# Kernel optimization log

Measured on AMD Instinct MI355X. Metric: run time of the kernel, lower is better.

The kernel has to match this reference:

```python
import jax, jax.numpy as jnp
import numpy as np
from jax import lax

MODEL_DIM = 384
KERNEL = 15
PAD = (KERNEL - 1) // 2
BATCH = 4096


def fake_quant(x, bits):
    """Per-tensor symmetric fake quantization with straight-through estimator.
    scale = max|x| / qmax, q = clip(round(x/scale), qmin, qmax), dq = q*scale.
    """
    qmax = float(2 ** (bits - 1) - 1)
    qmin = -float(2 ** (bits - 1))
    scale = jnp.maximum(jnp.max(jnp.abs(x)) / qmax, jnp.asarray(1e-8, x.dtype))
    dq = jnp.clip(jnp.round(x / scale), qmin, qmax) * scale
    return x + lax.stop_gradient(dq - x)  # STE: identity gradient


def setup_inputs() -> dict:
    key = jax.random.key(0)
    k = jax.random.split(key, 7)
    image = jax.random.normal(k[0], (BATCH, 28, 28), dtype=jnp.float32)
    # LinearQuant(28 -> model_dim)
    W1 = jax.random.normal(k[1], (MODEL_DIM, 28), dtype=jnp.float32) * (1.0 / np.sqrt(28))
    b1 = jax.random.normal(k[2], (MODEL_DIM,), dtype=jnp.float32) * 0.01
    # depthwise Conv1DQuant(model_dim, model_dim, K, groups=model_dim): weight [C_out, 1, K]
    Wc = jax.random.normal(k[3], (MODEL_DIM, 1, KERNEL), dtype=jnp.float32) * (1.0 / np.sqrt(KERNEL))
    bc = jax.random.normal(k[4], (MODEL_DIM,), dtype=jnp.float32) * 0.01
    # LinearQuant(28*model_dim -> 10)
    Wf = jax.random.normal(k[5], (10, 28 * MODEL_DIM), dtype=jnp.float32) * (1.0 / np.sqrt(28 * MODEL_DIM))
    bf = jax.random.normal(k[6], (10,), dtype=jnp.float32) * 0.01
    return {"image": image, "W1": W1, "b1": b1, "Wc": Wc, "bc": bc, "Wf": Wf, "bf": bf}


def reference(image, W1, b1, Wc, bc, Wf, bf):
    inp = image.reshape(-1, 28, 28)
    # linear_1 with 8-bit activation fake-quant in and 3-bit weight fake-quant
    x = fake_quant(inp, 8)
    lin = jnp.einsum('blf,of->blo', x, fake_quant(W1, 3)) + b1  # [B,28,model_dim]
    out1 = jnp.tanh(fake_quant(lin, 8))
    # depthwise conv1d over length 28, channels model_dim
    xc = jnp.transpose(fake_quant(out1, 8), (0, 2, 1))  # [B,C,L]
    conv = lax.conv_general_dilated(
        xc, fake_quant(Wc, 3), window_strides=(1,), padding=[(PAD, PAD)],
        dimension_numbers=('NCH', 'OIH', 'NCH'), feature_group_count=MODEL_DIM)
    conv = conv + bc[None, :, None]                      # [B,C,L]
    conv = jnp.transpose(conv, (0, 2, 1))                # [B,L,C]
    out2 = jnp.tanh(fake_quant(conv, 8)).reshape(-1, MODEL_DIM * 28)
    # final linear
    logits = fake_quant(out2, 8) @ fake_quant(Wf, 3).T + bf  # [B,10]
    return fake_quant(logits, 8)
```

## Files before the change

kernel.cpp:

```cpp
#include <hip/hip_runtime.h>

#define BATCH 4096
#define MD 384
#define KW 15
#define PADW 7
#define LSEQ 28
#define FIN 28

#define NX (BATCH*LSEQ*FIN)


#define B_SCF  0
#define B_LUT1 256
#define B_LUT2 512
#define B_PT0  1024
#define B_PT1  33792
#define B_PT2  41984
#define B_PTL  50176
#define B_W1B  54272
#define B_WCQ  78848
#define B_WFB  84992
#define B_LG   257024
#define B_XQB  420864

typedef __bf16 bf16x8 __attribute__((ext_vector_type(8)));
typedef float f32x4 __attribute__((ext_vector_type(4)));
typedef int i32x4 __attribute__((ext_vector_type(4)));

#if __has_builtin(__builtin_amdgcn_sdot4)
#define SDOT4(a,b,c) __builtin_amdgcn_sdot4((a),(b),(c),false)
#else
__device__ __forceinline__ int SDOT4(int a,int b,int c){
  c += ((a<<24)>>24)*((b<<24)>>24);
  c += ((a<<16)>>24)*((b<<16)>>24);
  c += ((a<<8)>>24)*((b<<8)>>24);
  c += (a>>24)*(b>>24);
  return c;
}
#endif

#if __has_builtin(__builtin_amdgcn_alignbyte)
#define ALIGNB(hi,lo,s) __builtin_amdgcn_alignbyte((hi),(lo),(s))
#else
#define ALIGNB(hi,lo,s) ((int)(((unsigned)(lo)>>(8*(s)))|((unsigned)(hi)<<(32-8*(s)))))
#endif

__device__ __forceinline__ unsigned short f2bf(float f){
  return (unsigned short)(__float_as_uint(f)>>16);
}

__device__ __forceinline__ unsigned lut_bperm(int iw,int lutw){
  int res=__builtin_amdgcn_ds_bpermute(iw,lutw);
  return ((unsigned)res>>(8*(iw&3)))&0xFFu;
}

__device__ __forceinline__ void blkStore4(float m0,float m1,float m2,float m3,float4* dst){
  #pragma unroll
  for(int off=32;off;off>>=1){
    m0=fmaxf(m0,__shfl_xor(m0,off,64));
    m1=fmaxf(m1,__shfl_xor(m1,off,64));
    m2=fmaxf(m2,__shfl_xor(m2,off,64));
    m3=fmaxf(m3,__shfl_xor(m3,off,64));
  }
  __shared__ float sm[4][4];
  int wid=threadIdx.x>>6;
  if((threadIdx.x&63)==0){sm[wid][0]=m0;sm[wid][1]=m1;sm[wid][2]=m2;sm[wid][3]=m3;}
  __syncthreads();
  if(threadIdx.x==0){
    for(int i=1;i<4;i++){
      m0=fmaxf(m0,sm[i][0]);m1=fmaxf(m1,sm[i][1]);
      m2=fmaxf(m2,sm[i][2]);m3=fmaxf(m3,sm[i][3]);
    }
    *dst=make_float4(m0,m1,m2,m3);
  }
}

__device__ __forceinline__ void blkStoreMM(float mn,float mx,float2* dst){
  #pragma unroll
  for(int off=32;off;off>>=1){
    mn=fminf(mn,__shfl_xor(mn,off,64));
    mx=fmaxf(mx,__shfl_xor(mx,off,64));
  }
  __shared__ float smn[8],smx[8];
  int wid=threadIdx.x>>6, nw=blockDim.x>>6;
  if((threadIdx.x&63)==0){smn[wid]=mn;smx[wid]=mx;}
  __syncthreads();
  if(threadIdx.x==0){
    for(int i=1;i<nw;i++){mn=fminf(mn,smn[i]);mx=fmaxf(mx,smx[i]);}
    *dst=make_float2(mn,mx);
  }
}

__global__ __launch_bounds__(256)
void k_maxabs_in(const float* __restrict__ img,const float* __restrict__ W1,
                 const float* __restrict__ Wc,const float* __restrict__ Wf,
                 float4* __restrict__ pt0){
  float m0=0.f,m1=0.f,m2=0.f,m3=0.f;
  const int N4=NX/4;
  const int NW1=MD*FIN, NWC=MD*KW, NWF=10*MD*LSEQ;
  const int total=N4+NW1+NWC+NWF;
  const float4* img4=(const float4*)img;
  for(int i=blockIdx.x*blockDim.x+threadIdx.x;i<total;i+=gridDim.x*blockDim.x){
    if(i<N4){
      float4 v=img4[i];
      m0=fmaxf(m0,fmaxf(fmaxf(fabsf(v.x),fabsf(v.y)),fmaxf(fabsf(v.z),fabsf(v.w))));
    }
    else if(i<N4+NW1) m1=fmaxf(m1,fabsf(W1[i-N4]));
    else if(i<N4+NW1+NWC) m2=fmaxf(m2,fabsf(Wc[i-N4-NW1]));
    else m3=fmaxf(m3,fabsf(Wf[i-N4-NW1-NWC]));
  }
  blkStore4(m0,m1,m2,m3,&pt0[blockIdx.x]);
}

__global__ __launch_bounds__(256)
void k_red0(const float4* __restrict__ pt,float* __restrict__ scf){
  int t=threadIdx.x;
  float m0=0.f,m1=0.f,m2=0.f,m3=0.f;
  for(int i=t;i<2048;i+=256){
    float4 v=pt[i];
    m0=fmaxf(m0,v.x);m1=fmaxf(m1,v.y);m2=fmaxf(m2,v.z);m3=fmaxf(m3,v.w);
  }
  #pragma unroll
  for(int off=32;off;off>>=1){
    m0=fmaxf(m0,__shfl_xor(m0,off,64));
    m1=fmaxf(m1,__shfl_xor(m1,off,64));
    m2=fmaxf(m2,__shfl_xor(m2,off,64));
    m3=fmaxf(m3,__shfl_xor(m3,off,64));
  }
  __shared__ float sm[4][4];
  int wid=t>>6;
  if((t&63)==0){sm[wid][0]=m0;sm[wid][1]=m1;sm[wid][2]=m2;sm[wid][3]=m3;}
  __syncthreads();
  if(t==0){
    for(int i=1;i<4;i++){
      m0=fmaxf(m0,sm[i][0]);m1=fmaxf(m1,sm[i][1]);
      m2=fmaxf(m2,sm[i][2]);m3=fmaxf(m3,sm[i][3]);
    }
    scf[0]=fmaxf(m0/127.f,1e-8f);
    scf[1]=fmaxf(m1/3.f,1e-8f);
    scf[2]=fmaxf(m2/3.f,1e-8f);
    scf[3]=fmaxf(m3/3.f,1e-8f);
  }
}

__global__ __launch_bounds__(256)
void k_redmm(const float2* __restrict__ pt,int n,float* __restrict__ scf,
             int preIdx,int outIdx,char* __restrict__ lutg){
  int t=threadIdx.x;
  float mn=1e30f,mx=-1e30f;
  for(int i=t;i<n;i+=256){
    float2 v=pt[i];
    mn=fminf(mn,v.x); mx=fmaxf(mx,v.y);
  }
  #pragma unroll
  for(int off=32;off;off>>=1){
    mn=fminf(mn,__shfl_xor(mn,off,64));
    mx=fmaxf(mx,__shfl_xor(mx,off,64));
  }
  __shared__ float smn[4],smx[4];
  __shared__ float bs,bso;
  int wid=t>>6;
  if((t&63)==0){smn[wid]=mn;smx[wid]=mx;}
  __syncthreads();
  if(t==0){
    for(int i=1;i<4;i++){mn=fminf(mn,smn[i]);mx=fmaxf(mx,smx[i]);}
    float ma=fmaxf(fabsf(mn),fabsf(mx));
    float s=fmaxf(ma/127.f,1e-8f);
    float a1=fabsf(fminf(fmaxf(rintf(mn/s),-128.f),127.f)*s);
    float a2=fabsf(fminf(fmaxf(rintf(mx/s),-128.f),127.f)*s);
    float so=fmaxf(tanhf(fmaxf(a1,a2))/127.f,1e-8f);
    scf[preIdx]=s; scf[outIdx]=so;
    bs=s; bso=so;
  }
  __syncthreads();
  float d=(float)(t-128)*bs;
  lutg[t]=(char)(int)fminf(fmaxf(rintf(tanhf(d)/bso),-128.f),127.f);
}

__global__ __launch_bounds__(256)
void k_prep(const float* __restrict__ img,const float* __restrict__ W1,
            const float* __restrict__ Wc,const float* __restrict__ Wf,
            const float* __restrict__ scf,char* __restrict__ wsb){
  float s_img=scf[0], s_w1=scf[1], s_wc=scf[2], s_wf=scf[3];
  float inv_img=1.f/s_img;
  unsigned short* xqb=(unsigned short*)(wsb+B_XQB);
  unsigned short* w1b=(unsigned short*)(wsb+B_W1B);
  char* wcpk=wsb+B_WCQ;
  char* wfb=wsb+B_WFB;
  const int T0=BATCH*LSEQ*32;
  const int T1=T0+MD*32;
  const int T2=T1+MD*16;
  const int T3=T2+10*10752;
  for(int i=blockIdx.x*blockDim.x+threadIdx.x;i<T3;i+=gridDim.x*blockDim.x){
    if(i<T0){
      int row=i>>5, cc=i&31;
      float q = cc<FIN ? fminf(fmaxf(rintf(img[row*FIN+cc]*inv_img),-128.f),127.f) : 0.f;
      xqb[i]=f2bf(q);
    } else if(i<T1){
      int j=i-T0; int o=j>>5, cc=j&31;
      float q = cc<FIN ? fminf(fmaxf(rintf(W1[o*FIN+cc]/s_w1),-4.f),3.f) : 0.f;
      w1b[j]=f2bf(q);
    } else if(i<T2){
      int j=i-T1; int c=j>>4, k=j&15;
      char q=0;
      if(k<KW) q=(char)(int)fminf(fmaxf(rintf(Wc[c*KW+k]/s_wc),-4.f),3.f);
      wcpk[j]=q;
    } else {
      int j=i-T2;
      int n=j/10752, r=j-n*10752;
      int c=r/28, l=r-c*28;
      wfb[j]=(char)(int)fminf(fmaxf(rintf(Wf[n*10752+l*MD+c]/s_wf),-4.f),3.f);
    }
  }
}

#define CWS 29
#define DWS 2692
template<int MODE>
__global__ __launch_bounds__(512)
void k_fused(const unsigned short* __restrict__ xqb,const unsigned short* __restrict__ w1b,
             const float* __restrict__ b1,const float* __restrict__ scf,
             const char* __restrict__ lut1g,const char* __restrict__ lut2g,
             const char* __restrict__ wcpk,const float* __restrict__ bc,
             const char* __restrict__ wfb,const float* __restrict__ bfv,
             float2* __restrict__ ptmm,float* __restrict__ lg,
             float* __restrict__ ptl){
  __shared__ int ldsI[MD*CWS];
  __shared__ int psumN[8][10][4];
  int t=threadIdx.x, wid=t>>6, lane=t&63, l4=lane>>4, l15=lane&15;
  {
    const int* src=(const int*)w1b;
    for(int i=t;i<6144;i+=512) ldsI[i]=src[i];
  }
  __syncthreads();
  unsigned short* Wlds=(unsigned short*)ldsI;
  bf16x8 bfr[3]; float b1v[3];
  #pragma unroll
  for(int ni=0;ni<3;ni++){
    int o=(wid*3+ni)*16+l15;
    bfr[ni]=*(const bf16x8*)&Wlds[o*32+l4*8];
    b1v[ni]=b1[o];
  }
  bf16x8 af[7];
  int r0=blockIdx.x*112;
  #pragma unroll
  for(int mt=0;mt<7;mt++)
    af[mt]=*(const bf16x8*)&xqb[(size_t)(r0+mt*16+l15)*32+l4*8];
  float sg=scf[0]*scf[1];
  float sgi=sg, b1s[3]={0.f,0.f,0.f};
  int lutA_w=0,lutB_w=0;
  float ck1=1.f,inv_cv=1.f,sfac=1.f,gsc=1.f;
  if constexpr(MODE>=1){
    float inv_lin=1.f/scf[4];
    sgi=sg*inv_lin;
    #pragma unroll
    for(int ni=0;ni<3;ni++) b1s[ni]=fmaf(b1v[ni],inv_lin,128.f);
    lutA_w=((const int*)lut1g)[lane];
    sfac=scf[5]*scf[2];
  }
  if constexpr(MODE==2){
    inv_cv=1.f/scf[6];
    ck1=sfac*inv_cv;
    gsc=scf[3]*scf[7];
    lutB_w=((const int*)lut2g)[lane];
  }
  if constexpr(MODE>=1) __syncthreads();

  f32x4 zero={0.f,0.f,0.f,0.f};
  float mn=1e30f,mx=-1e30f;
  float mnn[3]={1e30f,1e30f,1e30f},mxx[3]={-1e30f,-1e30f,-1e30f};
  #pragma unroll
  for(int ni=0;ni<3;ni++){
    int o=(wid*3+ni)*16+l15;
    #pragma unroll
    for(int mt=0;mt<7;mt++){
      f32x4 acc=__builtin_amdgcn_mfma_f32_16x16x32_bf16(af[mt],bfr[ni],zero,0,0,0);
      if constexpr(MODE==0){
        #pragma unroll
        for(int r=0;r<4;r++){
          mnn[ni]=fminf(mnn[ni],acc[r]); mxx[ni]=fmaxf(mxx[ni],acc[r]);
        }
      } else {
        unsigned w=0;
        #pragma unroll
        for(int r=0;r<4;r++){
          float x=fmaf(acc[r],sgi,b1s[ni]);
          int iw=(int)__builtin_amdgcn_fmed3f(rintf(x),0.f,255.f);
          w|=lut_bperm(iw,lutA_w)<<(8*r);
        }
        ldsI[o*CWS+mt*4+l4]=(int)w;
      }
    }
  }
  if constexpr(MODE==0){
    #pragma unroll
    for(int ni=0;ni<3;ni++){
      mn=fminf(mn,fmaf(mnn[ni],sg,b1v[ni]));
      mx=fmaxf(mx,fmaf(mxx[ni],sg,b1v[ni]));
    }
    blkStoreMM(mn,mx,&ptmm[blockIdx.x]);
    return;
  }
  __syncthreads();

  int oww[3][7];
  float mnc=1e30f,mxc=-1e30f;
  #pragma unroll
  for(int rr=0;rr<3;rr++){
    int j=t+rr*512;
    int s=j/384, c=j-s*384;
    i32x4 wq=*(const i32x4*)(wcpk+(size_t)c*16);
    float cbias=bc[c];
    float cq2=0.f;
    if constexpr(MODE==2) cq2=fmaf(cbias,inv_cv,128.f);
    int ext[11];
    ext[0]=0; ext[1]=0; ext[9]=0; ext[10]=0;
    #pragma unroll
    for(int i=0;i<7;i++) ext[2+i]=ldsI[c*CWS+s*7+i];
    int imn=0x7FFFFFFF,imx=0x80000000;
    #pragma unroll
    for(int l=0;l<LSEQ;l++){
      const int eb=l+1, bi=eb>>2, sh=eb&3;
      int A0,A1,A2,A3;
      if(sh==0){A0=ext[bi];A1=ext[bi+1];A2=ext[bi+2];A3=ext[bi+3];}
      else{
        A0=ALIGNB(ext[bi+1],ext[bi],sh);
        A1=ALIGNB(ext[bi+2],ext[bi+1],sh);
        A2=ALIGNB(ext[bi+3],ext[bi+2],sh);
        A3=ALIGNB(ext[bi+4],ext[bi+3],sh);
      }
      int idot=SDOT4(A0,wq[0],SDOT4(A1,wq[1],SDOT4(A2,wq[2],SDOT4(A3,wq[3],0))));
      if constexpr(MODE==1){
        imn=min(imn,idot); imx=max(imx,idot);
      } else {
        float x=fmaf((float)idot,ck1,cq2);
        int iw=(int)__builtin_amdgcn_fmed3f(rintf(x),0.f,255.f);
        unsigned q2=lut_bperm(iw,lutB_w);
        if((l&3)==0) oww[rr][l>>2]=(int)q2;
        else oww[rr][l>>2]|=(int)(q2<<(8*(l&3)));
      }
    }
    if constexpr(MODE==1){
      mnc=fminf(mnc,fmaf((float)imn,sfac,cbias));
      mxc=fmaxf(mxc,fmaf((float)imx,sfac,cbias));
    }
  }
  if constexpr(MODE==1){
    blkStoreMM(mnc,mxc,&ptmm[blockIdx.x]);
    return;
  }

  __syncthreads();
  #pragma unroll
  for(int rr=0;rr<3;rr++){
    int j=t+rr*512;
    int s=j/384, c=j-s*384;
    #pragma unroll
    for(int i=0;i<7;i++) ldsI[s*DWS+c*7+i]=oww[rr][i];
  }
  __syncthreads();

  {
    i32x4 acc={0,0,0,0};
    const char* ldsB=(const char*)ldsI;
    for(int kb=wid;kb<168;kb+=8){
      i32x4 a=*(const i32x4*)(ldsB+(size_t)(l15&3)*(DWS*4)+kb*64+l4*16);
      i32x4 b=*(const i32x4*)(wfb+(size_t)l15*10752+kb*64+l4*16);
      acc=__builtin_amdgcn_mfma_i32_16x16x64_i8(a,b,acc,0,0,0);
    }
    if(l4==0&&l15<10){
      #pragma unroll
      for(int r=0;r<4;r++) psumN[wid][l15][r]=acc[r];
    }
  }
  __syncthreads();
  float m=0.f;
  if(t<40){
    int s=t/10, o=t-s*10;
    int sum=0;
    #pragma unroll
    for(int w=0;w<8;w++) sum+=psumN[w][o][s];
    float v=fmaf((float)sum,gsc,bfv[o]);
    lg[(blockIdx.x*4+s)*10+o]=v;
    m=fabsf(v);
  }
  if(t<64){
    #pragma unroll
    for(int off=32;off;off>>=1) m=fmaxf(m,__shfl_xor(m,off,64));
    if(t==0) ptl[blockIdx.x]=m;
  }
}

__global__ __launch_bounds__(256)
void k_final(const float* __restrict__ lg,const float* __restrict__ ptl,
             float* __restrict__ out){
  int t=threadIdx.x;
  float m=0.f;
  for(int i=t;i<1024;i+=256) m=fmaxf(m,ptl[i]);
  #pragma unroll
  for(int off=32;off;off>>=1) m=fmaxf(m,__shfl_xor(m,off,64));
  __shared__ float sm[4];
  __shared__ float sv;
  int wid=t>>6;
  if((t&63)==0) sm[wid]=m;
  __syncthreads();
  if(t==0){
    for(int k=1;k<4;k++) m=fmaxf(m,sm[k]);
    sv=fmaxf(m/127.f,1e-8f);
  }
  __syncthreads();
  float s=sv;
  int i=blockIdx.x*256+t;
  out[i]=fminf(fmaxf(rintf(lg[i]/s),-128.f),127.f)*s;
}

extern "C" void kernel_launch(void* const* d_in, const int* in_sizes, int n_in,
                              void* d_out, int out_size, void* d_ws, size_t ws_size,
                              hipStream_t stream){
  const float* img=(const float*)d_in[0];
  const float* W1 =(const float*)d_in[1];
  const float* b1 =(const float*)d_in[2];
  const float* Wc =(const float*)d_in[3];
  const float* bc =(const float*)d_in[4];
  const float* Wf =(const float*)d_in[5];
  const float* bf =(const float*)d_in[6];
  float* out=(float*)d_out;
  char* wsb=(char*)d_ws;
  float* scf=(float*)(wsb+B_SCF);
  float4* pt0=(float4*)(wsb+B_PT0);
  float2* pt1=(float2*)(wsb+B_PT1);
  float2* pt2=(float2*)(wsb+B_PT2);
  float* ptl=(float*)(wsb+B_PTL);
  float* lg=(float*)(wsb+B_LG);
  const unsigned short* xqb=(const unsigned short*)(wsb+B_XQB);
  const unsigned short* w1b=(const unsigned short*)(wsb+B_W1B);
  const char* wcpk=wsb+B_WCQ;
  const char* wfb=wsb+B_WFB;

  k_maxabs_in<<<2048,256,0,stream>>>(img,W1,Wc,Wf,pt0);
  k_red0<<<1,256,0,stream>>>(pt0,scf);
  k_prep<<<4096,256,0,stream>>>(img,W1,Wc,Wf,scf,wsb);
  k_fused<0><<<1024,512,0,stream>>>(xqb,w1b,b1,scf,nullptr,nullptr,wcpk,bc,wfb,bf,pt1,nullptr,nullptr);
  k_redmm<<<1,256,0,stream>>>(pt1,1024,scf,4,5,wsb+B_LUT1);
  k_fused<1><<<1024,512,0,stream>>>(xqb,w1b,b1,scf,wsb+B_LUT1,nullptr,wcpk,bc,wfb,bf,pt2,nullptr,nullptr);
  k_redmm<<<1,256,0,stream>>>(pt2,1024,scf,6,7,wsb+B_LUT2);
  k_fused<2><<<1024,512,0,stream>>>(xqb,w1b,b1,scf,wsb+B_LUT1,wsb+B_LUT2,wcpk,bc,wfb,bf,nullptr,lg,ptl);
  k_final<<<160,256,0,stream>>>(lg,ptl,out);
}
```

Before: 105.6 us.

## Fold single-block reductions into consumer kernels and halve per-block batch tile

Removes the three single-block reduction kernels (k_red0, two k_redmm). Each consumer block now redoes the global min/max reduction over the partials itself and builds the tanh LUTs in shared memory. Each fused block now handles 2 samples (56 rows) instead of 4, doubling the grid to 2048 blocks and shrinking LDS use for higher occupancy. The trade is redundant reduction and LUT work in every block and lower MFMA utilisation per block, since 64 rows are computed for 56 used and only 2 of 4 result rows in the final matmul.

```diff
diff --git a/kernel.cpp b/kernel.cpp
--- a/kernel.cpp
+++ b/kernel.cpp
@@ -3,25 +3,21 @@
 #define BATCH 4096
 #define MD 384
 #define KW 15
-#define PADW 7
 #define LSEQ 28
 #define FIN 28
-
 #define NX (BATCH*LSEQ*FIN)
-
+#define NROWS (BATCH*LSEQ)
 
 #define B_SCF  0
-#define B_LUT1 256
-#define B_LUT2 512
 #define B_PT0  1024
 #define B_PT1  33792
-#define B_PT2  41984
-#define B_PTL  50176
-#define B_W1B  54272
-#define B_WCQ  78848
-#define B_WFB  84992
-#define B_LG   257024
-#define B_XQB  420864
+#define B_PT2  50176
+#define B_PTL  66560
+#define B_W1B  74752
+#define B_WCQ  99328
+#define B_WFB  105472
+#define B_LG   277504
+#define B_XQB  441344
 
 typedef __bf16 bf16x8 __attribute__((ext_vector_type(8)));
 typedef float f32x4 __attribute__((ext_vector_type(4)));
@@ -48,10 +44,18 @@
 __device__ __forceinline__ unsigned short f2bf(float f){
   return (unsigned short)(__float_as_uint(f)>>16);
 }
-
 __device__ __forceinline__ unsigned lut_bperm(int iw,int lutw){
   int res=__builtin_amdgcn_ds_bpermute(iw,lutw);
   return ((unsigned)res>>(8*(iw&3)))&0xFFu;
+}
+
+__device__ __forceinline__ void derive_scales(float mn,float mx,float* sp,float* so){
+  float ma=fmaxf(fabsf(mn),fabsf(mx));
+  float s=fmaxf(ma/127.f,1e-8f);
+  float a1=fabsf(fminf(fmaxf(rintf(mn/s),-128.f),127.f)*s);
+  float a2=fabsf(fminf(fmaxf(rintf(mx/s),-128.f),127.f)*s);
+  *sp=s;
+  *so=fmaxf(tanhf(fmaxf(a1,a2))/127.f,1e-8f);
 }
 
 __device__ __forceinline__ void blkStore4(float m0,float m1,float m2,float m3,float4* dst){
@@ -113,11 +117,14 @@
 }
 
 __global__ __launch_bounds__(256)
-void k_red0(const float4* __restrict__ pt,float* __restrict__ scf){
+void k_prep(const float* __restrict__ img,const float* __restrict__ W1,
+            const float* __restrict__ Wc,const float* __restrict__ Wf,
+            const float4* __restrict__ pt0,float* __restrict__ scf,
+            char* __restrict__ wsb){
   int t=threadIdx.x;
   float m0=0.f,m1=0.f,m2=0.f,m3=0.f;
   for(int i=t;i<2048;i+=256){
-    float4 v=pt[i];
+    float4 v=pt0[i];
     m0=fmaxf(m0,v.x);m1=fmaxf(m1,v.y);m2=fmaxf(m2,v.z);m3=fmaxf(m3,v.w);
   }
   #pragma unroll
@@ -128,6 +135,7 @@
     m3=fmaxf(m3,__shfl_xor(m3,off,64));
   }
   __shared__ float sm[4][4];
+  __shared__ float bs[4];
   int wid=t>>6;
   if((t&63)==0){sm[wid][0]=m0;sm[wid][1]=m1;sm[wid][2]=m2;sm[wid][3]=m3;}
   __syncthreads();
@@ -136,58 +144,20 @@
       m0=fmaxf(m0,sm[i][0]);m1=fmaxf(m1,sm[i][1]);
       m2=fmaxf(m2,sm[i][2]);m3=fmaxf(m3,sm[i][3]);
     }
-    scf[0]=fmaxf(m0/127.f,1e-8f);
-    scf[1]=fmaxf(m1/3.f,1e-8f);
-    scf[2]=fmaxf(m2/3.f,1e-8f);
-    scf[3]=fmaxf(m3/3.f,1e-8f);
-  }
-}
-
-__global__ __launch_bounds__(256)
-void k_redmm(const float2* __restrict__ pt,int n,float* __restrict__ scf,
-             int preIdx,int outIdx,char* __restrict__ lutg){
-  int t=threadIdx.x;
-  float mn=1e30f,mx=-1e30f;
-  for(int i=t;i<n;i+=256){
-    float2 v=pt[i];
-    mn=fminf(mn,v.x); mx=fmaxf(mx,v.y);
-  }
-  #pragma unroll
-  for(int off=32;off;off>>=1){
-    mn=fminf(mn,__shfl_xor(mn,off,64));
-    mx=fmaxf(mx,__shfl_xor(mx,off,64));
-  }
-  __shared__ float smn[4],smx[4];
-  __shared__ float bs,bso;
-  int wid=t>>6;
-  if((t&63)==0){smn[wid]=mn;smx[wid]=mx;}
-  __syncthreads();
-  if(t==0){
-    for(int i=1;i<4;i++){mn=fminf(mn,smn[i]);mx=fmaxf(mx,smx[i]);}
-    float ma=fmaxf(fabsf(mn),fabsf(mx));
-    float s=fmaxf(ma/127.f,1e-8f);
-    float a1=fabsf(fminf(fmaxf(rintf(mn/s),-128.f),127.f)*s);
-    float a2=fabsf(fminf(fmaxf(rintf(mx/s),-128.f),127.f)*s);
-    float so=fmaxf(tanhf(fmaxf(a1,a2))/127.f,1e-8f);
-    scf[preIdx]=s; scf[outIdx]=so;
-    bs=s; bso=so;
-  }
-  __syncthreads();
-  float d=(float)(t-128)*bs;
-  lutg[t]=(char)(int)fminf(fmaxf(rintf(tanhf(d)/bso),-128.f),127.f);
-}
-
-__global__ __launch_bounds__(256)
-void k_prep(const float* __restrict__ img,const float* __restrict__ W1,
-            const float* __restrict__ Wc,const float* __restrict__ Wf,
-            const float* __restrict__ scf,char* __restrict__ wsb){
-  float s_img=scf[0], s_w1=scf[1], s_wc=scf[2], s_wf=scf[3];
+    bs[0]=fmaxf(m0/127.f,1e-8f);
+    bs[1]=fmaxf(m1/3.f,1e-8f);
+    bs[2]=fmaxf(m2/3.f,1e-8f);
+    bs[3]=fmaxf(m3/3.f,1e-8f);
+    if(blockIdx.x==0){scf[0]=bs[0];scf[1]=bs[1];scf[2]=bs[2];scf[3]=bs[3];}
+  }
+  __syncthreads();
+  float s_img=bs[0], s_w1=bs[1], s_wc=bs[2], s_wf=bs[3];
   float inv_img=1.f/s_img;
   unsigned short* xqb=(unsigned short*)(wsb+B_XQB);
   unsigned short* w1b=(unsigned short*)(wsb+B_W1B);
   char* wcpk=wsb+B_WCQ;
   char* wfb=wsb+B_WFB;
-  const int T0=BATCH*LSEQ*32;
+  const int T0=NROWS*32;
   const int T1=T0+MD*32;
   const int T2=T1+MD*16;
   const int T3=T2+10*10752;
@@ -214,19 +184,22 @@
   }
 }
 
-#define CWS 29
-#define DWS 2692
+#define CWS 15
+#define DWSB 10768
 template<int MODE>
 __global__ __launch_bounds__(512)
 void k_fused(const unsigned short* __restrict__ xqb,const unsigned short* __restrict__ w1b,
              const float* __restrict__ b1,const float* __restrict__ scf,
-             const char* __restrict__ lut1g,const char* __restrict__ lut2g,
+             const float2* __restrict__ pt1,const float2* __restrict__ pt2,
              const char* __restrict__ wcpk,const float* __restrict__ bc,
              const char* __restrict__ wfb,const float* __restrict__ bfv,
-             float2* __restrict__ ptmm,float* __restrict__ lg,
+             float2* __restrict__ ptout,float* __restrict__ lg,
              float* __restrict__ ptl){
-  __shared__ int ldsI[MD*CWS];
-  __shared__ int psumN[8][10][4];
+  __shared__ int ldsI[6144];
+  __shared__ int psumN[8][10][2];
+  __shared__ char lutCA[256];
+  __shared__ char lutCB[256];
+  __shared__ float rs[2][8];
   int t=threadIdx.x, wid=t>>6, lane=t&63, l4=lane>>4, l15=lane&15;
   {
     const int* src=(const int*)w1b;
@@ -241,39 +214,85 @@
     bfr[ni]=*(const bf16x8*)&Wlds[o*32+l4*8];
     b1v[ni]=b1[o];
   }
-  bf16x8 af[7];
-  int r0=blockIdx.x*112;
-  #pragma unroll
-  for(int mt=0;mt<7;mt++)
-    af[mt]=*(const bf16x8*)&xqb[(size_t)(r0+mt*16+l15)*32+l4*8];
+  bf16x8 af[4];
+  int r0=blockIdx.x*56;
+  #pragma unroll
+  for(int mt=0;mt<4;mt++){
+    int rr=r0+mt*16+l15; rr=min(rr,NROWS-1);
+    af[mt]=*(const bf16x8*)&xqb[(size_t)rr*32+l4*8];
+  }
   float sg=scf[0]*scf[1];
   float sgi=sg, b1s[3]={0.f,0.f,0.f};
   int lutA_w=0,lutB_w=0;
   float ck1=1.f,inv_cv=1.f,sfac=1.f,gsc=1.f;
+  float s_lin=1.f,s_o1=1.f,s_cv=1.f,s_o2=1.f;
   if constexpr(MODE>=1){
-    float inv_lin=1.f/scf[4];
+    float mn1=1e30f,mx1=-1e30f;
+    for(int i=t;i<2048;i+=512){float2 v=pt1[i]; mn1=fminf(mn1,v.x); mx1=fmaxf(mx1,v.y);}
+    #pragma unroll
+    for(int off=32;off;off>>=1){
+      mn1=fminf(mn1,__shfl_xor(mn1,off,64));
+      mx1=fmaxf(mx1,__shfl_xor(mx1,off,64));
+    }
+    if(lane==0){rs[0][wid]=mn1; rs[1][wid]=mx1;}
+    __syncthreads();
+    mn1=rs[0][0]; mx1=rs[1][0];
+    #pragma unroll
+    for(int i=1;i<8;i++){mn1=fminf(mn1,rs[0][i]); mx1=fmaxf(mx1,rs[1][i]);}
+    derive_scales(mn1,mx1,&s_lin,&s_o1);
+    float inv_lin=1.f/s_lin;
     sgi=sg*inv_lin;
     #pragma unroll
     for(int ni=0;ni<3;ni++) b1s[ni]=fmaf(b1v[ni],inv_lin,128.f);
-    lutA_w=((const int*)lut1g)[lane];
-    sfac=scf[5]*scf[2];
+    sfac=s_o1*scf[2];
   }
   if constexpr(MODE==2){
-    inv_cv=1.f/scf[6];
+    float mn2=1e30f,mx2=-1e30f;
+    for(int i=t;i<2048;i+=512){float2 v=pt2[i]; mn2=fminf(mn2,v.x); mx2=fmaxf(mx2,v.y);}
+    #pragma unroll
+    for(int off=32;off;off>>=1){
+      mn2=fminf(mn2,__shfl_xor(mn2,off,64));
+      mx2=fmaxf(mx2,__shfl_xor(mx2,off,64));
+    }
+    __syncthreads();
+    if(lane==0){rs[0][wid]=mn2; rs[1][wid]=mx2;}
+    __syncthreads();
+    mn2=rs[0][0]; mx2=rs[1][0];
+    #pragma unroll
+    for(int i=1;i<8;i++){mn2=fminf(mn2,rs[0][i]); mx2=fmaxf(mx2,rs[1][i]);}
+    derive_scales(mn2,mx2,&s_cv,&s_o2);
+    inv_cv=1.f/s_cv;
     ck1=sfac*inv_cv;
-    gsc=scf[3]*scf[7];
-    lutB_w=((const int*)lut2g)[lane];
-  }
-  if constexpr(MODE>=1) __syncthreads();
+    gsc=scf[3]*s_o2;
+  }
+  if constexpr(MODE==1){
+    if(t<256){
+      float d=(float)(t-128)*s_lin;
+      lutCA[t]=(char)(int)fminf(fmaxf(rintf(tanhf(d)/s_o1),-128.f),127.f);
+    }
+  }
+  if constexpr(MODE==2){
+    if(t<256){
+      float d=(float)(t-128)*s_lin;
+      lutCA[t]=(char)(int)fminf(fmaxf(rintf(tanhf(d)/s_o1),-128.f),127.f);
+    } else {
+      float d=(float)(t-384)*s_cv;
+      lutCB[t-256]=(char)(int)fminf(fmaxf(rintf(tanhf(d)/s_o2),-128.f),127.f);
+    }
+  }
+  if constexpr(MODE>=1){
+    __syncthreads();
+    lutA_w=((const int*)lutCA)[lane];
+    if constexpr(MODE==2) lutB_w=((const int*)lutCB)[lane];
+  }
 
   f32x4 zero={0.f,0.f,0.f,0.f};
-  float mn=1e30f,mx=-1e30f;
   float mnn[3]={1e30f,1e30f,1e30f},mxx[3]={-1e30f,-1e30f,-1e30f};
   #pragma unroll
   for(int ni=0;ni<3;ni++){
     int o=(wid*3+ni)*16+l15;
     #pragma unroll
-    for(int mt=0;mt<7;mt++){
+    for(int mt=0;mt<4;mt++){
       f32x4 acc=__builtin_amdgcn_mfma_f32_16x16x32_bf16(af[mt],bfr[ni],zero,0,0,0);
       if constexpr(MODE==0){
         #pragma unroll
@@ -288,75 +307,84 @@
           int iw=(int)__builtin_amdgcn_fmed3f(rintf(x),0.f,255.f);
           w|=lut_bperm(iw,lutA_w)<<(8*r);
         }
-        ldsI[o*CWS+mt*4+l4]=(int)w;
+        int idx=mt*4+l4;
+        if(idx<14) ldsI[o*CWS+idx]=(int)w;
       }
     }
   }
   if constexpr(MODE==0){
+    float mn=1e30f,mx=-1e30f;
     #pragma unroll
     for(int ni=0;ni<3;ni++){
       mn=fminf(mn,fmaf(mnn[ni],sg,b1v[ni]));
       mx=fmaxf(mx,fmaf(mxx[ni],sg,b1v[ni]));
     }
-    blkStoreMM(mn,mx,&ptmm[blockIdx.x]);
+    blkStoreMM(mn,mx,&ptout[blockIdx.x]);
     return;
   }
   __syncthreads();
 
-  int oww[3][7];
+  int oww[2][7];
   float mnc=1e30f,mxc=-1e30f;
   #pragma unroll
-  for(int rr=0;rr<3;rr++){
+  for(int rr=0;rr<2;rr++){
     int j=t+rr*512;
-    int s=j/384, c=j-s*384;
-    i32x4 wq=*(const i32x4*)(wcpk+(size_t)c*16);
-    float cbias=bc[c];
-    float cq2=0.f;
-    if constexpr(MODE==2) cq2=fmaf(cbias,inv_cv,128.f);
-    int ext[11];
-    ext[0]=0; ext[1]=0; ext[9]=0; ext[10]=0;
-    #pragma unroll
-    for(int i=0;i<7;i++) ext[2+i]=ldsI[c*CWS+s*7+i];
-    int imn=0x7FFFFFFF,imx=0x80000000;
-    #pragma unroll
-    for(int l=0;l<LSEQ;l++){
-      const int eb=l+1, bi=eb>>2, sh=eb&3;
-      int A0,A1,A2,A3;
-      if(sh==0){A0=ext[bi];A1=ext[bi+1];A2=ext[bi+2];A3=ext[bi+3];}
-      else{
-        A0=ALIGNB(ext[bi+1],ext[bi],sh);
-        A1=ALIGNB(ext[bi+2],ext[bi+1],sh);
-        A2=ALIGNB(ext[bi+3],ext[bi+2],sh);
-        A3=ALIGNB(ext[bi+4],ext[bi+3],sh);
+    if(j<768){
+      int s=j>>8>=1?(j>=384?1:0):(j>=384?1:0);
+      s=(j>=384)?1:0;
+      int c=j-s*384;
+      i32x4 wq=*(const i32x4*)(wcpk+(size_t)c*16);
+      float cbias=bc[c];
+      float cq2=0.f;
+      if constexpr(MODE==2) cq2=fmaf(cbias,inv_cv,128.f);
+      int ext[11];
+      ext[0]=0; ext[1]=0; ext[9]=0; ext[10]=0;
+      #pragma unroll
+      for(int i=0;i<7;i++) ext[2+i]=ldsI[c*CWS+s*7+i];
+      int imn=0x7FFFFFFF,imx=0x80000000;
+      #pragma unroll
+      for(int l=0;l<LSEQ;l++){
+        const int eb=l+1, bi=eb>>2, sh=eb&3;
+        int A0,A1,A2,A3;
+        if(sh==0){A0=ext[bi];A1=ext[bi+1];A2=ext[bi+2];A3=ext[bi+3];}
+        else{
+          A0=ALIGNB(ext[bi+1],ext[bi],sh);
+          A1=ALIGNB(ext[bi+2],ext[bi+1],sh);
+          A2=ALIGNB(ext[bi+3],ext[bi+2],sh);
+          A3=ALIGNB(ext[bi+4],ext[bi+3],sh);
+        }
+        int idot=SDOT4(A0,wq[0],SDOT4(A1,wq[1],SDOT4(A2,wq[2],SDOT4(A3,wq[3],0))));
+        if constexpr(MODE==1){
+          imn=min(imn,idot); imx=max(imx,idot);
+        } else {
+          float x=fmaf((float)idot,ck1,cq2);
+          int iw=(int)__builtin_amdgcn_fmed3f(rintf(x),0.f,255.f);
+          unsigned q2=lut_bperm(iw,lutB_w);
+          if((l&3)==0) oww[rr][l>>2]=(int)q2;
+          else oww[rr][l>>2]|=(int)(q2<<(8*(l&3)));
+        }
       }
-      int idot=SDOT4(A0,wq[0],SDOT4(A1,wq[1],SDOT4(A2,wq[2],SDOT4(A3,wq[3],0))));
       if constexpr(MODE==1){
-        imn=min(imn,idot); imx=max(imx,idot);
-      } else {
-        float x=fmaf((float)idot,ck1,cq2);
-        int iw=(int)__builtin_amdgcn_fmed3f(rintf(x),0.f,255.f);
-        unsigned q2=lut_bperm(iw,lutB_w);
-        if((l&3)==0) oww[rr][l>>2]=(int)q2;
-        else oww[rr][l>>2]|=(int)(q2<<(8*(l&3)));
+        mnc=fminf(mnc,fmaf((float)imn,sfac,cbias));
+        mxc=fmaxf(mxc,fmaf((float)imx,sfac,cbias));
       }
     }
-    if constexpr(MODE==1){
-      mnc=fminf(mnc,fmaf((float)imn,sfac,cbias));
-      mxc=fmaxf(mxc,fmaf((float)imx,sfac,cbias));
-    }
   }
   if constexpr(MODE==1){
-    blkStoreMM(mnc,mxc,&ptmm[blockIdx.x]);
+    blkStoreMM(mnc,mxc,&ptout[blockIdx.x]);
     return;
   }
 
   __syncthreads();
   #pragma unroll
-  for(int rr=0;rr<3;rr++){
+  for(int rr=0;rr<2;rr++){
     int j=t+rr*512;
-    int s=j/384, c=j-s*384;
-    #pragma unroll
-    for(int i=0;i<7;i++) ldsI[s*DWS+c*7+i]=oww[rr][i];
+    if(j<768){
+      int s=(j>=384)?1:0;
+      int c=j-s*384;
+      #pragma unroll
+      for(int i=0;i<7;i++) ldsI[s*(DWSB/4)+c*7+i]=oww[rr][i];
+    }
   }
   __syncthreads();
 
@@ -364,24 +392,24 @@
     i32x4 acc={0,0,0,0};
     const char* ldsB=(const char*)ldsI;
     for(int kb=wid;kb<168;kb+=8){
-      i32x4 a=*(const i32x4*)(ldsB+(size_t)(l15&3)*(DWS*4)+kb*64+l4*16);
+      i32x4 a=*(const i32x4*)(ldsB+(size_t)(l15&1)*DWSB+kb*64+l4*16);
       i32x4 b=*(const i32x4*)(wfb+(size_t)l15*10752+kb*64+l4*16);
       acc=__builtin_amdgcn_mfma_i32_16x16x64_i8(a,b,acc,0,0,0);
     }
     if(l4==0&&l15<10){
-      #pragma unroll
-      for(int r=0;r<4;r++) psumN[wid][l15][r]=acc[r];
+      psumN[wid][l15][0]=acc[0];
+      psumN[wid][l15][1]=acc[1];
     }
   }
   __syncthreads();
   float m=0.f;
-  if(t<40){
+  if(t<20){
     int s=t/10, o=t-s*10;
     int sum=0;
     #pragma unroll
     for(int w=0;w<8;w++) sum+=psumN[w][o][s];
     float v=fmaf((float)sum,gsc,bfv[o]);
-    lg[(blockIdx.x*4+s)*10+o]=v;
+    lg[(blockIdx.x*2+s)*10+o]=v;
     m=fabsf(v);
   }
   if(t<64){
@@ -396,7 +424,7 @@
              float* __restrict__ out){
   int t=threadIdx.x;
   float m=0.f;
-  for(int i=t;i<1024;i+=256) m=fmaxf(m,ptl[i]);
+  for(int i=t;i<2048;i+=256) m=fmaxf(m,ptl[i]);
   #pragma unroll
   for(int off=32;off;off>>=1) m=fmaxf(m,__shfl_xor(m,off,64));
   __shared__ float sm[4];
@@ -438,12 +466,9 @@
   const char* wfb=wsb+B_WFB;
 
   k_maxabs_in<<<2048,256,0,stream>>>(img,W1,Wc,Wf,pt0);
-  k_red0<<<1,256,0,stream>>>(pt0,scf);
-  k_prep<<<4096,256,0,stream>>>(img,W1,Wc,Wf,scf,wsb);
-  k_fused<0><<<1024,512,0,stream>>>(xqb,w1b,b1,scf,nullptr,nullptr,wcpk,bc,wfb,bf,pt1,nullptr,nullptr);
-  k_redmm<<<1,256,0,stream>>>(pt1,1024,scf,4,5,wsb+B_LUT1);
-  k_fused<1><<<1024,512,0,stream>>>(xqb,w1b,b1,scf,wsb+B_LUT1,nullptr,wcpk,bc,wfb,bf,pt2,nullptr,nullptr);
-  k_redmm<<<1,256,0,stream>>>(pt2,1024,scf,6,7,wsb+B_LUT2);
-  k_fused<2><<<1024,512,0,stream>>>(xqb,w1b,b1,scf,wsb+B_LUT1,wsb+B_LUT2,wcpk,bc,wfb,bf,nullptr,lg,ptl);
+  k_prep<<<2048,256,0,stream>>>(img,W1,Wc,Wf,pt0,scf,wsb);
+  k_fused<0><<<2048,512,0,stream>>>(xqb,w1b,b1,scf,nullptr,nullptr,wcpk,bc,wfb,bf,pt1,nullptr,nullptr);
+  k_fused<1><<<2048,512,0,stream>>>(xqb,w1b,b1,scf,pt1,nullptr,wcpk,bc,wfb,bf,pt2,nullptr,nullptr);
+  k_fused<2><<<2048,512,0,stream>>>(xqb,w1b,b1,scf,pt1,pt2,wcpk,bc,wfb,bf,nullptr,lg,ptl);
   k_final<<<160,256,0,stream>>>(lg,ptl,out);
 }
```

Result: slower. 135.4 us (+28.3%).

## Process three samples per fused block to shrink LDS and raise occupancy

Applied to the files above, without the earlier changes.

Each fused block now handles 3 samples (84 rows) instead of 4 (112 rows), so the grid grows from 1024 to 1366 blocks. The LDS stride per channel drops from 29 to 23 ints, which cuts shared memory per block and could let more blocks be resident per CU. The cost is extra guard logic, clamped tail rows, some wasted MFMA lanes (6 row tiles with only 84 valid rows, and a fourth A-row duplicated), and more partial results for the reductions to combine.

```diff
diff --git a/kernel.cpp b/kernel.cpp
--- a/kernel.cpp
+++ b/kernel.cpp
@@ -3,25 +3,25 @@
 #define BATCH 4096
 #define MD 384
 #define KW 15
-#define PADW 7
 #define LSEQ 28
 #define FIN 28
-
 #define NX (BATCH*LSEQ*FIN)
-
+#define NROWS (BATCH*LSEQ)
+#define SAMP 3
+#define NB 1366
 
 #define B_SCF  0
 #define B_LUT1 256
 #define B_LUT2 512
 #define B_PT0  1024
 #define B_PT1  33792
-#define B_PT2  41984
-#define B_PTL  50176
-#define B_W1B  54272
-#define B_WCQ  78848
-#define B_WFB  84992
-#define B_LG   257024
-#define B_XQB  420864
+#define B_PT2  50176
+#define B_PTL  66560
+#define B_W1B  74752
+#define B_WCQ  99328
+#define B_WFB  105472
+#define B_LG   277504
+#define B_XQB  441344
 
 typedef __bf16 bf16x8 __attribute__((ext_vector_type(8)));
 typedef float f32x4 __attribute__((ext_vector_type(4)));
@@ -48,7 +48,6 @@
 __device__ __forceinline__ unsigned short f2bf(float f){
   return (unsigned short)(__float_as_uint(f)>>16);
 }
-
 __device__ __forceinline__ unsigned lut_bperm(int iw,int lutw){
   int res=__builtin_amdgcn_ds_bpermute(iw,lutw);
   return ((unsigned)res>>(8*(iw&3)))&0xFFu;
@@ -187,7 +186,7 @@
   unsigned short* w1b=(unsigned short*)(wsb+B_W1B);
   char* wcpk=wsb+B_WCQ;
   char* wfb=wsb+B_WFB;
-  const int T0=BATCH*LSEQ*32;
+  const int T0=NROWS*32;
   const int T1=T0+MD*32;
   const int T2=T1+MD*16;
   const int T3=T2+10*10752;
@@ -214,7 +213,7 @@
   }
 }
 
-#define CWS 29
+#define CWS 23
 #define DWS 2692
 template<int MODE>
 __global__ __launch_bounds__(512)
@@ -241,11 +240,14 @@
     bfr[ni]=*(const bf16x8*)&Wlds[o*32+l4*8];
     b1v[ni]=b1[o];
   }
-  bf16x8 af[7];
-  int r0=blockIdx.x*112;
-  #pragma unroll
-  for(int mt=0;mt<7;mt++)
-    af[mt]=*(const bf16x8*)&xqb[(size_t)(r0+mt*16+l15)*32+l4*8];
+  bf16x8 af[6];
+  int r0=blockIdx.x*84;
+  #pragma unroll
+  for(int mt=0;mt<6;mt++){
+    int rr_=r0+mt*16+l15; rr_=min(rr_,NROWS-1);
+    af[mt]=*(const bf16x8*)&xqb[(size_t)rr_*32+l4*8];
+  }
+  int vs=BATCH-blockIdx.x*SAMP;
   float sg=scf[0]*scf[1];
   float sgi=sg, b1s[3]={0.f,0.f,0.f};
   int lutA_w=0,lutB_w=0;
@@ -267,13 +269,12 @@
   if constexpr(MODE>=1) __syncthreads();
 
   f32x4 zero={0.f,0.f,0.f,0.f};
-  float mn=1e30f,mx=-1e30f;
   float mnn[3]={1e30f,1e30f,1e30f},mxx[3]={-1e30f,-1e30f,-1e30f};
   #pragma unroll
   for(int ni=0;ni<3;ni++){
     int o=(wid*3+ni)*16+l15;
     #pragma unroll
-    for(int mt=0;mt<7;mt++){
+    for(int mt=0;mt<6;mt++){
       f32x4 acc=__builtin_amdgcn_mfma_f32_16x16x32_bf16(af[mt],bfr[ni],zero,0,0,0);
       if constexpr(MODE==0){
         #pragma unroll
@@ -288,11 +289,13 @@
           int iw=(int)__builtin_amdgcn_fmed3f(rintf(x),0.f,255.f);
           w|=lut_bperm(iw,lutA_w)<<(8*r);
         }
-        ldsI[o*CWS+mt*4+l4]=(int)w;
+        int idx=mt*4+l4;
+        if(idx<21) ldsI[o*CWS+idx]=(int)w;
       }
     }
   }
   if constexpr(MODE==0){
+    float mn=1e30f,mx=-1e30f;
     #pragma unroll
     for(int ni=0;ni<3;ni++){
       mn=fminf(mn,fmaf(mnn[ni],sg,b1v[ni]));
@@ -308,41 +311,45 @@
   #pragma unroll
   for(int rr=0;rr<3;rr++){
     int j=t+rr*512;
-    int s=j/384, c=j-s*384;
-    i32x4 wq=*(const i32x4*)(wcpk+(size_t)c*16);
-    float cbias=bc[c];
-    float cq2=0.f;
-    if constexpr(MODE==2) cq2=fmaf(cbias,inv_cv,128.f);
-    int ext[11];
-    ext[0]=0; ext[1]=0; ext[9]=0; ext[10]=0;
-    #pragma unroll
-    for(int i=0;i<7;i++) ext[2+i]=ldsI[c*CWS+s*7+i];
-    int imn=0x7FFFFFFF,imx=0x80000000;
-    #pragma unroll
-    for(int l=0;l<LSEQ;l++){
-      const int eb=l+1, bi=eb>>2, sh=eb&3;
-      int A0,A1,A2,A3;
-      if(sh==0){A0=ext[bi];A1=ext[bi+1];A2=ext[bi+2];A3=ext[bi+3];}
-      else{
-        A0=ALIGNB(ext[bi+1],ext[bi],sh);
-        A1=ALIGNB(ext[bi+2],ext[bi+1],sh);
-        A2=ALIGNB(ext[bi+3],ext[bi+2],sh);
-        A3=ALIGNB(ext[bi+4],ext[bi+3],sh);
+    if(j<SAMP*MD){
+      int s=j/MD, c=j-s*MD;
+      i32x4 wq=*(const i32x4*)(wcpk+(size_t)c*16);
+      float cbias=bc[c];
+      float cq2=0.f;
+      if constexpr(MODE==2) cq2=fmaf(cbias,inv_cv,128.f);
+      int ext[11];
+      ext[0]=0; ext[1]=0; ext[9]=0; ext[10]=0;
+      #pragma unroll
+      for(int i=0;i<7;i++) ext[2+i]=ldsI[c*CWS+s*7+i];
+      int imn=0x7FFFFFFF,imx=0x80000000;
+      #pragma unroll
+      for(int l=0;l<LSEQ;l++){
+        const int eb=l+1, bi=eb>>2, sh=eb&3;
+        int A0,A1,A2,A3;
+        if(sh==0){A0=ext[bi];A1=ext[bi+1];A2=ext[bi+2];A3=ext[bi+3];}
+        else{
+          A0=ALIGNB(ext[bi+1],ext[bi],sh);
+          A1=ALIGNB(ext[bi+2],ext[bi+1],sh);
+          A2=ALIGNB(ext[bi+3],ext[bi+2],sh);
+          A3=ALIGNB(ext[bi+4],ext[bi+3],sh);
+        }
+        int idot=SDOT4(A0,wq[0],SDOT4(A1,wq[1],SDOT4(A2,wq[2],SDOT4(A3,wq[3],0))));
+        if constexpr(MODE==1){
+          imn=min(imn,idot); imx=max(imx,idot);
+        } else {
+          float x=fmaf((float)idot,ck1,cq2);
+          int iw=(int)__builtin_amdgcn_fmed3f(rintf(x),0.f,255.f);
+          unsigned q2=lut_bperm(iw,lutB_w);
+          if((l&3)==0) oww[rr][l>>2]=(int)q2;
+          else oww[rr][l>>2]|=(int)(q2<<(8*(l&3)));
+        }
       }
-      int idot=SDOT4(A0,wq[0],SDOT4(A1,wq[1],SDOT4(A2,wq[2],SDOT4(A3,wq[3],0))));
       if constexpr(MODE==1){
-        imn=min(imn,idot); imx=max(imx,idot);
-      } else {
-        float x=fmaf((float)idot,ck1,cq2);
-        int iw=(int)__builtin_amdgcn_fmed3f(rintf(x),0.f,255.f);
-        unsigned q2=lut_bperm(iw,lutB_w);
-        if((l&3)==0) oww[rr][l>>2]=(int)q2;
-        else oww[rr][l>>2]|=(int)(q2<<(8*(l&3)));
+        if(s<vs){
+          mnc=fminf(mnc,fmaf((float)imn,sfac,cbias));
+          mxc=fmaxf(mxc,fmaf((float)imx,sfac,cbias));
+        }
       }
-    }
-    if constexpr(MODE==1){
-      mnc=fminf(mnc,fmaf((float)imn,sfac,cbias));
-      mxc=fmaxf(mxc,fmaf((float)imx,sfac,cbias));
     }
   }
   if constexpr(MODE==1){
@@ -354,17 +361,20 @@
   #pragma unroll
   for(int rr=0;rr<3;rr++){
     int j=t+rr*512;
-    int s=j/384, c=j-s*384;
-    #pragma unroll
-    for(int i=0;i<7;i++) ldsI[s*DWS+c*7+i]=oww[rr][i];
+    if(j<SAMP*MD){
+      int s=j/MD, c=j-s*MD;
+      #pragma unroll
+      for(int i=0;i<7;i++) ldsI[s*DWS+c*7+i]=oww[rr][i];
+    }
   }
   __syncthreads();
 
   {
     i32x4 acc={0,0,0,0};
     const char* ldsB=(const char*)ldsI;
+    int ar=l15&3; if(ar>2) ar=2;
     for(int kb=wid;kb<168;kb+=8){
-      i32x4 a=*(const i32x4*)(ldsB+(size_t)(l15&3)*(DWS*4)+kb*64+l4*16);
+      i32x4 a=*(const i32x4*)(ldsB+(size_t)ar*(DWS*4)+kb*64+l4*16);
       i32x4 b=*(const i32x4*)(wfb+(size_t)l15*10752+kb*64+l4*16);
       acc=__builtin_amdgcn_mfma_i32_16x16x64_i8(a,b,acc,0,0,0);
     }
@@ -375,14 +385,16 @@
   }
   __syncthreads();
   float m=0.f;
-  if(t<40){
+  if(t<30){
     int s=t/10, o=t-s*10;
-    int sum=0;
-    #pragma unroll
-    for(int w=0;w<8;w++) sum+=psumN[w][o][s];
-    float v=fmaf((float)sum,gsc,bfv[o]);
-    lg[(blockIdx.x*4+s)*10+o]=v;
-    m=fabsf(v);
+    if(blockIdx.x*SAMP+s<BATCH){
+      int sum=0;
+      #pragma unroll
+      for(int w=0;w<8;w++) sum+=psumN[w][o][s];
+      float v=fmaf((float)sum,gsc,bfv[o]);
+      lg[(size_t)(blockIdx.x*SAMP+s)*10+o]=v;
+      m=fabsf(v);
+    }
   }
   if(t<64){
     #pragma unroll
@@ -396,7 +408,7 @@
              float* __restrict__ out){
   int t=threadIdx.x;
   float m=0.f;
-  for(int i=t;i<1024;i+=256) m=fmaxf(m,ptl[i]);
+  for(int i=t;i<NB;i+=256) m=fmaxf(m,ptl[i]);
   #pragma unroll
   for(int off=32;off;off>>=1) m=fmaxf(m,__shfl_xor(m,off,64));
   __shared__ float sm[4];
@@ -440,10 +452,10 @@
   k_maxabs_in<<<2048,256,0,stream>>>(img,W1,Wc,Wf,pt0);
   k_red0<<<1,256,0,stream>>>(pt0,scf);
   k_prep<<<4096,256,0,stream>>>(img,W1,Wc,Wf,scf,wsb);
-  k_fused<0><<<1024,512,0,stream>>>(xqb,w1b,b1,scf,nullptr,nullptr,wcpk,bc,wfb,bf,pt1,nullptr,nullptr);
-  k_redmm<<<1,256,0,stream>>>(pt1,1024,scf,4,5,wsb+B_LUT1);
-  k_fused<1><<<1024,512,0,stream>>>(xqb,w1b,b1,scf,wsb+B_LUT1,nullptr,wcpk,bc,wfb,bf,pt2,nullptr,nullptr);
-  k_redmm<<<1,256,0,stream>>>(pt2,1024,scf,6,7,wsb+B_LUT2);
-  k_fused<2><<<1024,512,0,stream>>>(xqb,w1b,b1,scf,wsb+B_LUT1,wsb+B_LUT2,wcpk,bc,wfb,bf,nullptr,lg,ptl);
+  k_fused<0><<<NB,512,0,stream>>>(xqb,w1b,b1,scf,nullptr,nullptr,wcpk,bc,wfb,bf,pt1,nullptr,nullptr);
+  k_redmm<<<1,256,0,stream>>>(pt1,NB,scf,4,5,wsb+B_LUT1);
+  k_fused<1><<<NB,512,0,stream>>>(xqb,w1b,b1,scf,wsb+B_LUT1,nullptr,wcpk,bc,wfb,bf,pt2,nullptr,nullptr);
+  k_redmm<<<1,256,0,stream>>>(pt2,NB,scf,6,7,wsb+B_LUT2);
+  k_fused<2><<<NB,512,0,stream>>>(xqb,w1b,b1,scf,wsb+B_LUT1,wsb+B_LUT2,wcpk,bc,wfb,bf,nullptr,lg,ptl);
   k_final<<<160,256,0,stream>>>(lg,ptl,out);
 }
```

Measured after the change: 131.0 us. +24.1%, slower.
